# Performance work log

Hardware: AMD Instinct MI355X
Metric: run time of the kernel (lower is better)

## Reference

```python
import jax, jax.numpy as jnp
import numpy as np

IGNORE_INDEX = -100
BETA = 0.1

B, T, H, V = 4, 512, 1024, 32000  # sequences, tokens/seq, hidden, vocab


def setup_inputs() -> dict:
    key = jax.random.key(0)
    ks = jax.random.split(key, 9)
    scale = 1.0 / np.sqrt(H)
    return {
        "_input": jax.random.normal(ks[0], (B * T, H), jnp.float32),
        "weight": jax.random.normal(ks[1], (V, H), jnp.float32) * scale,
        "target": jax.random.randint(ks[2], (B * T,), 0, V, jnp.int64),
        "bias": jax.random.normal(ks[3], (V,), jnp.float32) * 0.01,
        "preference_labels": jax.random.bernoulli(ks[4], 0.5, (B,)),
        "ref_input": jax.random.normal(ks[5], (B * T, H), jnp.float32),
        "ref_weight": jax.random.normal(ks[6], (V, H), jnp.float32) * scale,
        "ref_bias": jax.random.normal(ks[7], (V,), jnp.float32) * 0.01,
        "kl": jax.random.uniform(ks[8], (1,), jnp.float32),
    }


def _seq_log_prob(x, w, b, target):
    # x: (B*T, H), w: (V, H), b: (V,) -> per-sequence summed target logprob (B,)
    logits = x @ w.T + b  # (B*T, V) -- the tensor the fused kernel avoids
    logp = jax.nn.log_softmax(logits, axis=-1)
    safe_tgt = jnp.clip(target, 0, logp.shape[-1] - 1)
    tok_logp = jnp.take_along_axis(logp, safe_tgt[:, None], axis=-1)[:, 0]
    mask = target != IGNORE_INDEX
    tok_logp = jnp.where(mask, tok_logp, 0.0).reshape(B, T)
    return tok_logp.sum(axis=-1)  # average_log_prob=False


def reference(_input, weight, target, bias, preference_labels, ref_input, ref_weight, ref_bias, kl):
    pol_logp = _seq_log_prob(_input, weight, bias, target)          # (B,)
    ref_logp = _seq_log_prob(ref_input, ref_weight, ref_bias, target)  # (B,)
    logratios = pol_logp - ref_logp
    multiplier = jnp.where(preference_labels, 1.0, -1.0)
    losses = 1.0 - jax.nn.sigmoid(BETA * (logratios - kl[0]) * multiplier)
    loss = losses.sum() / target.shape[0]  # divide by full_target.shape[0] = B*T
    rewards = BETA * logratios
    chosen_rewards_sum = (rewards * preference_labels).sum()
    rejected_rewards_sum = (rewards * (~preference_labels)).sum()
    return loss, chosen_rewards_sum, rejected_rewards_sum
```

## Files before the change

kernel.cpp:

```cpp
#include <hip/hip_runtime.h>

#define BT    2048
#define HDIM  1024
#define VDIM  32000
#define NSEQ  4
#define BETA  0.1f
#define IGNORE_IDX (-100)

typedef __attribute__((ext_vector_type(8))) short bf16x8;
typedef __attribute__((ext_vector_type(8))) unsigned short u16x8;
typedef __attribute__((ext_vector_type(4))) float f32x4;

#define WS_BF_BYTE  32768
#define XBF_OFF     0
#define XRBF_OFF    (BT * HDIM)
#define WBF_OFF     (2 * BT * HDIM)
#define WRBF_OFF    (2 * BT * HDIM + VDIM * HDIM)
#define CVT_TOTAL   (2 * BT * HDIM + 2 * VDIM * HDIM)
#define WS_NEED     ((size_t)WS_BF_BYTE + (size_t)CVT_TOTAL * 2)

__device__ __forceinline__ unsigned short f2bf_rne(float f) {
  unsigned int u = __builtin_bit_cast(unsigned int, f);
  u += 0x7fffu + ((u >> 16) & 1u);
  return (unsigned short)(u >> 16);
}

__device__ __forceinline__ u16x8 cvt8(float4 a, float4 b) {
  u16x8 v;
  v[0] = f2bf_rne(a.x); v[1] = f2bf_rne(a.y); v[2] = f2bf_rne(a.z); v[3] = f2bf_rne(a.w);
  v[4] = f2bf_rne(b.x); v[5] = f2bf_rne(b.y); v[6] = f2bf_rne(b.z); v[7] = f2bf_rne(b.w);
  return v;
}

__global__ __launch_bounds__(256) void kto_zero_ws(float* p) {
  p[blockIdx.x * 256 + threadIdx.x] = 0.0f;
}

__global__ __launch_bounds__(256) void kto_convert(
    const float* __restrict__ X, const float* __restrict__ Xr,
    const float* __restrict__ W, const float* __restrict__ Wr,
    unsigned short* __restrict__ bf)
{
  size_t gid8 = ((size_t)blockIdx.x * 256 + threadIdx.x) * 8;
  if (gid8 >= (size_t)CVT_TOTAL) return;
  const float* src; size_t off;
  if (gid8 < (size_t)XRBF_OFF)      { src = X;  off = gid8; }
  else if (gid8 < (size_t)WBF_OFF)  { src = Xr; off = gid8 - XRBF_OFF; }
  else if (gid8 < (size_t)WRBF_OFF) { src = W;  off = gid8 - WBF_OFF; }
  else                              { src = Wr; off = gid8 - WRBF_OFF; }
  const float4* p = (const float4*)(src + off);
  float4 a = p[0], b = p[1];
  *(u16x8*)(bf + gid8) = cvt8(a, b);
}

#define GLD16(g, l) __builtin_amdgcn_global_load_lds( \
    (const __attribute__((address_space(1))) unsigned int*)(g), \
    (__attribute__((address_space(3))) unsigned int*)(l), 16, 0, 0)

__global__ __launch_bounds__(256) void kto_lse_gemm_fast(
    const unsigned short* __restrict__ bf,
    const float* __restrict__ Bp, const float* __restrict__ Br,
    const int* __restrict__ target,
    float* __restrict__ ws_se, float* __restrict__ ws_tg)
{
  const int model = blockIdx.z;
  const unsigned short* __restrict__ Xb = bf + (model ? XRBF_OFF : XBF_OFF);
  const unsigned short* __restrict__ Wb = bf + (model ? WRBF_OFF : WBF_OFF);
  const float* __restrict__ Bv = model ? Br : Bp;

  __shared__ unsigned short Asm[128 * 32];
  __shared__ unsigned short Bsm[128 * 32];

  const int tid  = threadIdx.x;
  const int wave = tid >> 6;
  const int lane = tid & 63;
  const int q    = lane >> 4;
  const int c    = lane & 15;
  const int mW   = (wave >> 1) * 64;
  const int nW   = (wave & 1) * 64;
  const int mBase = blockIdx.x * 128;
  const int nBase = blockIdx.y * 128;

  const int lrow = lane >> 2;
  const int lchk = (lane & 3) ^ ((lane >> 3) & 3);

  const char* gsrc[4];
  unsigned short* ldst[4];
  #pragma unroll
  for (int j = 0; j < 4; ++j) {
    const int seg = wave * 4 + j;
    if (seg < 8) {
      const int row = mBase + seg * 16 + lrow;
      gsrc[j] = (const char*)Xb + (size_t)row * (HDIM * 2) + lchk * 16;
      ldst[j] = &Asm[seg * 512];
    } else {
      const int row = nBase + (seg - 8) * 16 + lrow;
      gsrc[j] = (const char*)Wb + (size_t)row * (HDIM * 2) + lchk * 16;
      ldst[j] = &Bsm[(seg - 8) * 512];
    }
  }

  const int swz = (q ^ ((c >> 1) & 3)) * 8;

  f32x4 acc[4][4] = {};

  for (int kt = 0; kt < HDIM / 32; ++kt) {
    __syncthreads();
    const size_t kb = (size_t)kt * 64;
    #pragma unroll
    for (int j = 0; j < 4; ++j)
      GLD16(gsrc[j] + kb, ldst[j]);
    __syncthreads();

    bf16x8 afr[4], bfr[4];
    #pragma unroll
    for (int mi = 0; mi < 4; ++mi)
      afr[mi] = *(const bf16x8*)&Asm[(mW + mi * 16 + c) * 32 + swz];
    #pragma unroll
    for (int ni = 0; ni < 4; ++ni)
      bfr[ni] = *(const bf16x8*)&Bsm[(nW + ni * 16 + c) * 32 + swz];
    #pragma unroll
    for (int mi = 0; mi < 4; ++mi)
      #pragma unroll
      for (int ni = 0; ni < 4; ++ni)
        acc[mi][ni] = __builtin_amdgcn_mfma_f32_16x16x32_bf16(afr[mi], bfr[ni], acc[mi][ni], 0, 0, 0);
  }

  float se_acc[4][4] = {};
  float tg_acc[4][4] = {};
  int tgt_idx[4][4];
  #pragma unroll
  for (int mi = 0; mi < 4; ++mi)
    #pragma unroll
    for (int r = 0; r < 4; ++r)
      tgt_idx[mi][r] = target[mBase + mW + mi * 16 + q * 4 + r];

  #pragma unroll
  for (int ni = 0; ni < 4; ++ni) {
    const int col = nBase + nW + ni * 16 + c;
    const float bv = Bv[col];
    #pragma unroll
    for (int mi = 0; mi < 4; ++mi)
      #pragma unroll
      for (int r = 0; r < 4; ++r) {
        float logit = acc[mi][ni][r] + bv;
        se_acc[mi][r] += __expf(logit);
        if (tgt_idx[mi][r] == col) tg_acc[mi][r] += logit;
      }
  }

  #pragma unroll
  for (int mi = 0; mi < 4; ++mi)
    #pragma unroll
    for (int r = 0; r < 4; ++r) {
      float s = se_acc[mi][r];
      float t = tg_acc[mi][r];
      #pragma unroll
      for (int off = 1; off < 16; off <<= 1) {
        s += __shfl_xor(s, off, 64);
        t += __shfl_xor(t, off, 64);
      }
      if (c == ((mi << 2) | r)) {
        const int row = mBase + mW + mi * 16 + q * 4 + r;
        atomicAdd(&ws_se[model * BT + row], s);
        atomicAdd(&ws_tg[model * BT + row], t);
      }
    }
}

#define SBM 128
#define SBN 128
#define SBK 32
#define SVSLICE 1280
#define SNITER  (SVSLICE / SBN)
#define SKTILES (HDIM / SBK)
#define SLDK    (SBK + 8)

__device__ __forceinline__ void cvt_store8s(unsigned short* dst, float4 a, float4 b) {
  *(u16x8*)dst = cvt8(a, b);
}

__global__ __launch_bounds__(256) void kto_lse_gemm_slow(
    const float* __restrict__ Xp, const float* __restrict__ Wp, const float* __restrict__ Bp,
    const float* __restrict__ Xr, const float* __restrict__ Wr, const float* __restrict__ Br,
    const int* __restrict__ target, float* __restrict__ ws_se, float* __restrict__ ws_tg)
{
  const int model = blockIdx.z;
  const float* __restrict__ X  = model ? Xr : Xp;
  const float* __restrict__ W  = model ? Wr : Wp;
  const float* __restrict__ Bv = model ? Br : Bp;

  __shared__ unsigned short Asm[SBM][SLDK];
  __shared__ unsigned short Bsm[SBN][SLDK];

  const int tid  = threadIdx.x;
  const int wave = tid >> 6;
  const int lane = tid & 63;
  const int q    = lane >> 4;
  const int c    = lane & 15;
  const int mW   = (wave >> 1) * 64;
  const int nW   = (wave & 1) * 64;
  const int mBase = blockIdx.x * SBM;
  const int vBase = blockIdx.y * SVSLICE;

  const int srow = tid >> 1;
  const int scol = (tid & 1) << 4;

  int tgt_idx[4][4];
  #pragma unroll
  for (int mi = 0; mi < 4; ++mi)
    #pragma unroll
    for (int r = 0; r < 4; ++r)
      tgt_idx[mi][r] = target[mBase + mW + mi * 16 + q * 4 + r];

  float se_acc[4][4] = {};
  float tg_acc[4][4] = {};

  for (int it = 0; it < SNITER; ++it) {
    const int nIterBase = vBase + it * SBN;
    f32x4 acc[4][4] = {};

    for (int kt = 0; kt < SKTILES; ++kt) {
      __syncthreads();
      {
        const float4* a4 = (const float4*)(X + (size_t)(mBase + srow) * HDIM + kt * SBK + scol);
        float4 a0 = a4[0], a1 = a4[1], a2 = a4[2], a3 = a4[3];
        const float4* b4 = (const float4*)(W + (size_t)(nIterBase + srow) * HDIM + kt * SBK + scol);
        float4 b0 = b4[0], b1 = b4[1], b2 = b4[2], b3 = b4[3];
        cvt_store8s(&Asm[srow][scol],     a0, a1);
        cvt_store8s(&Asm[srow][scol + 8], a2, a3);
        cvt_store8s(&Bsm[srow][scol],     b0, b1);
        cvt_store8s(&Bsm[srow][scol + 8], b2, b3);
      }
      __syncthreads();

      bf16x8 afr[4], bfr[4];
      #pragma unroll
      for (int mi = 0; mi < 4; ++mi)
        afr[mi] = *(const bf16x8*)&Asm[mW + mi * 16 + c][q * 8];
      #pragma unroll
      for (int ni = 0; ni < 4; ++ni)
        bfr[ni] = *(const bf16x8*)&Bsm[nW + ni * 16 + c][q * 8];
      #pragma unroll
      for (int mi = 0; mi < 4; ++mi)
        #pragma unroll
        for (int ni = 0; ni < 4; ++ni)
          acc[mi][ni] = __builtin_amdgcn_mfma_f32_16x16x32_bf16(afr[mi], bfr[ni], acc[mi][ni], 0, 0, 0);
    }

    #pragma unroll
    for (int ni = 0; ni < 4; ++ni) {
      const int col = nIterBase + nW + ni * 16 + c;
      const float bv = Bv[col];
      #pragma unroll
      for (int mi = 0; mi < 4; ++mi)
        #pragma unroll
        for (int r = 0; r < 4; ++r) {
          float logit = acc[mi][ni][r] + bv;
          se_acc[mi][r] += __expf(logit);
          if (tgt_idx[mi][r] == col) tg_acc[mi][r] += logit;
        }
    }
  }

  #pragma unroll
  for (int mi = 0; mi < 4; ++mi)
    #pragma unroll
    for (int r = 0; r < 4; ++r) {
      float s = se_acc[mi][r];
      float t = tg_acc[mi][r];
      #pragma unroll
      for (int off = 1; off < 16; off <<= 1) {
        s += __shfl_xor(s, off, 64);
        t += __shfl_xor(t, off, 64);
      }
      if (c == 0) {
        const int row = mBase + mW + mi * 16 + q * 4 + r;
        atomicAdd(&ws_se[model * BT + row], s);
        atomicAdd(&ws_tg[model * BT + row], t);
      }
    }
}

__global__ __launch_bounds__(256) void kto_finalize(
    const float* __restrict__ ws_se, const float* __restrict__ ws_tg,
    const int* __restrict__ target, const int* __restrict__ pref,
    const float* __restrict__ kl, float* __restrict__ out)
{
  __shared__ float lr[NSEQ];
  const int tid = threadIdx.x;
  if (tid < NSEQ) lr[tid] = 0.0f;
  __syncthreads();
  for (int t = tid; t < BT; t += 256) {
    float d = 0.0f;
    if (target[t] != IGNORE_IDX) {
      float lp_p = ws_tg[t]      - __logf(ws_se[t]);
      float lp_r = ws_tg[BT + t] - __logf(ws_se[BT + t]);
      d = lp_p - lp_r;
    }
    atomicAdd(&lr[t >> 9], d);
  }
  __syncthreads();
  if (tid == 0) {
    float loss = 0.f, ch = 0.f, rj = 0.f;
    const float klv = kl[0];
    for (int b = 0; b < NSEQ; ++b) {
      float logratio = lr[b];
      bool p = pref[b] != 0;
      float mult = p ? 1.0f : -1.0f;
      float z = BETA * (logratio - klv) * mult;
      float sig = 1.0f / (1.0f + __expf(-z));
      loss += 1.0f - sig;
      float rw = BETA * logratio;
      if (p) ch += rw; else rj += rw;
    }
    out[0] = loss / (float)BT;
    out[1] = ch;
    out[2] = rj;
  }
}

extern "C" void kernel_launch(void* const* d_in, const int* in_sizes, int n_in,
                              void* d_out, int out_size, void* d_ws, size_t ws_size,
                              hipStream_t stream) {
  (void)in_sizes; (void)n_in; (void)out_size;
  const float* X    = (const float*)d_in[0];
  const float* W    = (const float*)d_in[1];
  const int*   tgt  = (const int*)d_in[2];
  const float* bias = (const float*)d_in[3];
  const int*   pref = (const int*)d_in[4];
  const float* Xr   = (const float*)d_in[5];
  const float* Wr   = (const float*)d_in[6];
  const float* br   = (const float*)d_in[7];
  const float* kl   = (const float*)d_in[8];
  float* out = (float*)d_out;

  float* ws_se = (float*)d_ws;
  float* ws_tg = ws_se + 2 * BT;

  kto_zero_ws<<<32, 256, 0, stream>>>(ws_se);

  if (ws_size >= WS_NEED) {
    unsigned short* bf = (unsigned short*)((char*)d_ws + WS_BF_BYTE);
    kto_convert<<<(CVT_TOTAL / 2048), 256, 0, stream>>>(X, Xr, W, Wr, bf);
    dim3 grid(BT / 128, VDIM / 128, 2);
    kto_lse_gemm_fast<<<grid, 256, 0, stream>>>(bf, bias, br, tgt, ws_se, ws_tg);
  } else {
    dim3 grid(BT / SBM, VDIM / SVSLICE, 2);
    kto_lse_gemm_slow<<<grid, 256, 0, stream>>>(X, W, bias, Xr, Wr, br, tgt, ws_se, ws_tg);
  }

  kto_finalize<<<1, 256, 0, stream>>>(ws_se, ws_tg, tgt, pref, kl, out);
}
```

Measured before the change: 668.5 us.

## Double GEMM K-tile, remap blocks to XCDs, fold zeroing into convert

The fast GEMM now loads K=64 per iteration with an 8-chunk XOR swizzle, which halves the number of barrier pairs per tile. It also uses a 1D grid whose block index is decoded so each XCD handles one model and one quadrant of the tile space, to improve L2 locality. The convert kernel processes 16 elements per thread and zeroes the accumulation workspace in block 0, removing a separate launch. This relies on block 0 zeroing finishing before the GEMM atomics, which stream ordering guarantees, and it doubles LDS use per block.

Measured after the change: 748.8 us. +12.0%, slower.

```diff
diff --git a/kernel.cpp b/kernel.cpp
--- a/kernel.cpp
+++ b/kernel.cpp
@@ -32,44 +32,54 @@
   return v;
 }
 
-__global__ __launch_bounds__(256) void kto_zero_ws(float* p) {
-  p[blockIdx.x * 256 + threadIdx.x] = 0.0f;
-}
-
 __global__ __launch_bounds__(256) void kto_convert(
     const float* __restrict__ X, const float* __restrict__ Xr,
     const float* __restrict__ W, const float* __restrict__ Wr,
-    unsigned short* __restrict__ bf)
+    unsigned short* __restrict__ bf, float* __restrict__ ws_zero)
 {
-  size_t gid8 = ((size_t)blockIdx.x * 256 + threadIdx.x) * 8;
-  if (gid8 >= (size_t)CVT_TOTAL) return;
+  if (blockIdx.x == 0) {
+    for (int i = threadIdx.x; i < 4 * BT; i += 256) ws_zero[i] = 0.0f;
+  }
+  size_t gid = ((size_t)blockIdx.x * 256 + threadIdx.x) * 16;
+  if (gid >= (size_t)CVT_TOTAL) return;
   const float* src; size_t off;
-  if (gid8 < (size_t)XRBF_OFF)      { src = X;  off = gid8; }
-  else if (gid8 < (size_t)WBF_OFF)  { src = Xr; off = gid8 - XRBF_OFF; }
-  else if (gid8 < (size_t)WRBF_OFF) { src = W;  off = gid8 - WBF_OFF; }
-  else                              { src = Wr; off = gid8 - WRBF_OFF; }
+  if (gid < (size_t)XRBF_OFF)      { src = X;  off = gid; }
+  else if (gid < (size_t)WBF_OFF)  { src = Xr; off = gid - XRBF_OFF; }
+  else if (gid < (size_t)WRBF_OFF) { src = W;  off = gid - WBF_OFF; }
+  else                             { src = Wr; off = gid - WRBF_OFF; }
   const float4* p = (const float4*)(src + off);
-  float4 a = p[0], b = p[1];
-  *(u16x8*)(bf + gid8) = cvt8(a, b);
+  float4 a = p[0], b = p[1], c = p[2], d = p[3];
+  *(u16x8*)(bf + gid)     = cvt8(a, b);
+  *(u16x8*)(bf + gid + 8) = cvt8(c, d);
 }
 
 #define GLD16(g, l) __builtin_amdgcn_global_load_lds( \
     (const __attribute__((address_space(1))) unsigned int*)(g), \
     (__attribute__((address_space(3))) unsigned int*)(l), 16, 0, 0)
 
-__global__ __launch_bounds__(256) void kto_lse_gemm_fast(
+__global__ __launch_bounds__(256) void kto_lse_gemm3(
     const unsigned short* __restrict__ bf,
     const float* __restrict__ Bp, const float* __restrict__ Br,
     const int* __restrict__ target,
     float* __restrict__ ws_se, float* __restrict__ ws_tg)
 {
-  const int model = blockIdx.z;
+  const int b    = blockIdx.x;
+  const int xcd  = b & 7;
+  const int j    = b >> 3;
+  const int model = xcd >> 2;
+  const int k2   = xcd & 3;
+  const int xt   = (k2 & 1) * 8 + (j & 7);
+  const int yt   = ((k2 >> 1) & 1) * 125 + (j >> 3);
+
   const unsigned short* __restrict__ Xb = bf + (model ? XRBF_OFF : XBF_OFF);
   const unsigned short* __restrict__ Wb = bf + (model ? WRBF_OFF : WBF_OFF);
   const float* __restrict__ Bv = model ? Br : Bp;
 
-  __shared__ unsigned short Asm[128 * 32];
-  __shared__ unsigned short Bsm[128 * 32];
+  const int mBase = xt * 128;
+  const int nBase = yt * 128;
+
+  __shared__ unsigned short Asm[128 * 64];
+  __shared__ unsigned short Bsm[128 * 64];
 
   const int tid  = threadIdx.x;
   const int wave = tid >> 6;
@@ -78,52 +88,56 @@
   const int c    = lane & 15;
   const int mW   = (wave >> 1) * 64;
   const int nW   = (wave & 1) * 64;
-  const int mBase = blockIdx.x * 128;
-  const int nBase = blockIdx.y * 128;
-
-  const int lrow = lane >> 2;
-  const int lchk = (lane & 3) ^ ((lane >> 3) & 3);
-
-  const char* gsrc[4];
-  unsigned short* ldst[4];
-  #pragma unroll
-  for (int j = 0; j < 4; ++j) {
-    const int seg = wave * 4 + j;
-    if (seg < 8) {
-      const int row = mBase + seg * 16 + lrow;
-      gsrc[j] = (const char*)Xb + (size_t)row * (HDIM * 2) + lchk * 16;
-      ldst[j] = &Asm[seg * 512];
-    } else {
-      const int row = nBase + (seg - 8) * 16 + lrow;
-      gsrc[j] = (const char*)Wb + (size_t)row * (HDIM * 2) + lchk * 16;
-      ldst[j] = &Bsm[(seg - 8) * 512];
-    }
-  }
-
-  const int swz = (q ^ ((c >> 1) & 3)) * 8;
+
+  const int lrow = lane >> 3;
+  const int lchk = (lane & 7) ^ (lrow & 7);
+
+  const char* gsrcA[4]; const char* gsrcB[4];
+  unsigned short* ldstA[4]; unsigned short* ldstB[4];
+  #pragma unroll
+  for (int s = 0; s < 4; ++s) {
+    const int seg = wave * 4 + s;
+    const int rowA = mBase + seg * 8 + lrow;
+    const int rowB = nBase + seg * 8 + lrow;
+    gsrcA[s] = (const char*)Xb + (size_t)rowA * (HDIM * 2) + lchk * 16;
+    gsrcB[s] = (const char*)Wb + (size_t)rowB * (HDIM * 2) + lchk * 16;
+    ldstA[s] = &Asm[seg * 512];
+    ldstB[s] = &Bsm[seg * 512];
+  }
 
   f32x4 acc[4][4] = {};
 
-  for (int kt = 0; kt < HDIM / 32; ++kt) {
+  for (int kt = 0; kt < HDIM / 64; ++kt) {
     __syncthreads();
-    const size_t kb = (size_t)kt * 64;
-    #pragma unroll
-    for (int j = 0; j < 4; ++j)
-      GLD16(gsrc[j] + kb, ldst[j]);
+    const size_t kb = (size_t)kt * 128;
+    #pragma unroll
+    for (int s = 0; s < 4; ++s) {
+      GLD16(gsrcA[s] + kb, ldstA[s]);
+      GLD16(gsrcB[s] + kb, ldstB[s]);
+    }
     __syncthreads();
 
-    bf16x8 afr[4], bfr[4];
-    #pragma unroll
-    for (int mi = 0; mi < 4; ++mi)
-      afr[mi] = *(const bf16x8*)&Asm[(mW + mi * 16 + c) * 32 + swz];
-    #pragma unroll
-    for (int ni = 0; ni < 4; ++ni)
-      bfr[ni] = *(const bf16x8*)&Bsm[(nW + ni * 16 + c) * 32 + swz];
-    #pragma unroll
-    for (int mi = 0; mi < 4; ++mi)
-      #pragma unroll
-      for (int ni = 0; ni < 4; ++ni)
-        acc[mi][ni] = __builtin_amdgcn_mfma_f32_16x16x32_bf16(afr[mi], bfr[ni], acc[mi][ni], 0, 0, 0);
+    #pragma unroll
+    for (int h = 0; h < 2; ++h) {
+      bf16x8 afr[4], bfr[4];
+      #pragma unroll
+      for (int mi = 0; mi < 4; ++mi) {
+        const int row = mW + mi * 16 + c;
+        const int slot = ((h << 2) | q) ^ (row & 7);
+        afr[mi] = *(const bf16x8*)&Asm[row * 64 + slot * 8];
+      }
+      #pragma unroll
+      for (int ni = 0; ni < 4; ++ni) {
+        const int row = nW + ni * 16 + c;
+        const int slot = ((h << 2) | q) ^ (row & 7);
+        bfr[ni] = *(const bf16x8*)&Bsm[row * 64 + slot * 8];
+      }
+      #pragma unroll
+      for (int mi = 0; mi < 4; ++mi)
+        #pragma unroll
+        for (int ni = 0; ni < 4; ++ni)
+          acc[mi][ni] = __builtin_amdgcn_mfma_f32_16x16x32_bf16(afr[mi], bfr[ni], acc[mi][ni], 0, 0, 0);
+    }
   }
 
   float se_acc[4][4] = {};
@@ -168,16 +182,10 @@
     }
 }
 
-#define SBM 128
-#define SBN 128
-#define SBK 32
-#define SVSLICE 1280
-#define SNITER  (SVSLICE / SBN)
-#define SKTILES (HDIM / SBK)
-#define SLDK    (SBK + 8)
-
-__device__ __forceinline__ void cvt_store8s(unsigned short* dst, float4 a, float4 b) {
-  *(u16x8*)dst = cvt8(a, b);
+#define SLDK 40
+
+__global__ __launch_bounds__(256) void kto_zero_ws(float* p) {
+  p[blockIdx.x * 256 + threadIdx.x] = 0.0f;
 }
 
 __global__ __launch_bounds__(256) void kto_lse_gemm_slow(
@@ -190,8 +198,8 @@
   const float* __restrict__ W  = model ? Wr : Wp;
   const float* __restrict__ Bv = model ? Br : Bp;
 
-  __shared__ unsigned short Asm[SBM][SLDK];
-  __shared__ unsigned short Bsm[SBN][SLDK];
+  __shared__ unsigned short Asm[128][SLDK];
+  __shared__ unsigned short Bsm[128][SLDK];
 
   const int tid  = threadIdx.x;
   const int wave = tid >> 6;
@@ -200,8 +208,8 @@
   const int c    = lane & 15;
   const int mW   = (wave >> 1) * 64;
   const int nW   = (wave & 1) * 64;
-  const int mBase = blockIdx.x * SBM;
-  const int vBase = blockIdx.y * SVSLICE;
+  const int mBase = blockIdx.x * 128;
+  const int vBase = blockIdx.y * 1280;
 
   const int srow = tid >> 1;
   const int scol = (tid & 1) << 4;
@@ -216,24 +224,22 @@
   float se_acc[4][4] = {};
   float tg_acc[4][4] = {};
 
-  for (int it = 0; it < SNITER; ++it) {
-    const int nIterBase = vBase + it * SBN;
+  for (int it = 0; it < 10; ++it) {
+    const int nIterBase = vBase + it * 128;
     f32x4 acc[4][4] = {};
-
-    for (int kt = 0; kt < SKTILES; ++kt) {
+    for (int kt = 0; kt < HDIM / 32; ++kt) {
       __syncthreads();
       {
-        const float4* a4 = (const float4*)(X + (size_t)(mBase + srow) * HDIM + kt * SBK + scol);
+        const float4* a4 = (const float4*)(X + (size_t)(mBase + srow) * HDIM + kt * 32 + scol);
         float4 a0 = a4[0], a1 = a4[1], a2 = a4[2], a3 = a4[3];
-        const float4* b4 = (const float4*)(W + (size_t)(nIterBase + srow) * HDIM + kt * SBK + scol);
+        const float4* b4 = (const float4*)(W + (size_t)(nIterBase + srow) * HDIM + kt * 32 + scol);
         float4 b0 = b4[0], b1 = b4[1], b2 = b4[2], b3 = b4[3];
-        cvt_store8s(&Asm[srow][scol],     a0, a1);
-        cvt_store8s(&Asm[srow][scol + 8], a2, a3);
-        cvt_store8s(&Bsm[srow][scol],     b0, b1);
-        cvt_store8s(&Bsm[srow][scol + 8], b2, b3);
+        *(u16x8*)&Asm[srow][scol]     = cvt8(a0, a1);
+        *(u16x8*)&Asm[srow][scol + 8] = cvt8(a2, a3);
+        *(u16x8*)&Bsm[srow][scol]     = cvt8(b0, b1);
+        *(u16x8*)&Bsm[srow][scol + 8] = cvt8(b2, b3);
       }
       __syncthreads();
-
       bf16x8 afr[4], bfr[4];
       #pragma unroll
       for (int mi = 0; mi < 4; ++mi)
@@ -247,7 +253,6 @@
         for (int ni = 0; ni < 4; ++ni)
           acc[mi][ni] = __builtin_amdgcn_mfma_f32_16x16x32_bf16(afr[mi], bfr[ni], acc[mi][ni], 0, 0, 0);
     }
-
     #pragma unroll
     for (int ni = 0; ni < 4; ++ni) {
       const int col = nIterBase + nW + ni * 16 + c;
@@ -262,7 +267,6 @@
         }
     }
   }
-
   #pragma unroll
   for (int mi = 0; mi < 4; ++mi)
     #pragma unroll
@@ -338,15 +342,13 @@
   float* ws_se = (float*)d_ws;
   float* ws_tg = ws_se + 2 * BT;
 
-  kto_zero_ws<<<32, 256, 0, stream>>>(ws_se);
-
   if (ws_size >= WS_NEED) {
     unsigned short* bf = (unsigned short*)((char*)d_ws + WS_BF_BYTE);
-    kto_convert<<<(CVT_TOTAL / 2048), 256, 0, stream>>>(X, Xr, W, Wr, bf);
-    dim3 grid(BT / 128, VDIM / 128, 2);
-    kto_lse_gemm_fast<<<grid, 256, 0, stream>>>(bf, bias, br, tgt, ws_se, ws_tg);
+    kto_convert<<<(CVT_TOTAL / 4096), 256, 0, stream>>>(X, Xr, W, Wr, bf, ws_se);
+    kto_lse_gemm3<<<8000, 256, 0, stream>>>(bf, bias, br, tgt, ws_se, ws_tg);
   } else {
-    dim3 grid(BT / SBM, VDIM / SVSLICE, 2);
+    kto_zero_ws<<<32, 256, 0, stream>>>(ws_se);
+    dim3 grid(BT / 128, VDIM / 1280, 2);
     kto_lse_gemm_slow<<<grid, 256, 0, stream>>>(X, W, bias, Xr, Wr, br, tgt, ws_se, ws_tg);
   }
 
```
